# Kernel optimization log

Hardware: AMD Instinct MI355X
Metric: run time of the kernel (lower is better)

## Reference

```python
import jax, jax.numpy as jnp
import numpy as np

T, B, I_DIM, H_DIM = 256, 64, 1024, 1024


def setup_inputs() -> dict:
    key = jax.random.key(0)
    k_in, k_wx, k_wh = jax.random.split(key, 3)
    # xavier-normal-ish scale for [hidden, input] matrices
    std_x = float(np.sqrt(2.0 / (I_DIM + H_DIM)))
    std_h = float(np.sqrt(2.0 / (H_DIM + H_DIM)))
    return {
        "inputs": jax.random.normal(k_in, (T, B, I_DIM), dtype=jnp.float32),
        "W_x": jax.random.normal(k_wx, (4, H_DIM, I_DIM), dtype=jnp.float32) * std_x,
        "W_h": jax.random.normal(k_wh, (4, H_DIM, H_DIM), dtype=jnp.float32) * std_h,
        "bias": jnp.zeros((4, H_DIM), dtype=jnp.float32),
        "mask_x": jnp.ones((4, H_DIM, I_DIM), dtype=jnp.float32),
        "mask_h": jnp.ones((4, H_DIM, H_DIM), dtype=jnp.float32),
        "H0": jnp.zeros((B, H_DIM), dtype=jnp.float32),
        "C0": jnp.zeros((B, H_DIM), dtype=jnp.float32),
    }


def reference(inputs, W_x, W_h, bias, mask_x, mask_h, H0, C0):
    # masked + transposed weights: (4, in_dim, hidden) so X @ W works
    Wx_t = jnp.transpose(W_x * mask_x, (0, 2, 1))  # (4, I, H)
    Wh_t = jnp.transpose(W_h * mask_h, (0, 2, 1))  # (4, H, H)

    # gate order per original indexing: 0=i, 1=f, 2=o, 3=c
    def step(carry, X):
        H, C = carry
        # fused gate GEMMs: (4, B, H)
        g = (jnp.einsum('bi,gih->gbh', X, Wx_t)
             + jnp.einsum('bh,ghk->gbk', H, Wh_t)
             + bias[:, None, :])
        I_g = jax.nn.sigmoid(g[0])
        F_g = jax.nn.sigmoid(g[1])
        O_g = jax.nn.sigmoid(g[2])
        C_t = jnp.tanh(g[3])
        C_new = F_g * C + I_g * C_t
        H_new = O_g * jnp.tanh(C_new)
        return (H_new, C_new), H_new

    (_, _), outputs = jax.lax.scan(step, (H0, C0), inputs)
    return outputs  # (T, B, H)
```

## Files before the change

kernel.cpp:

```cpp
#include <hip/hip_runtime.h>

typedef __attribute__((ext_vector_type(8))) short short8;
typedef __attribute__((ext_vector_type(4))) float floatx4;

#define T_STEPS 256
#define BATCH   64
#define IDIM    1024
#define HDIM    1024
#define KDIM    (IDIM + HDIM)
#define MB      16
#define HB      16
#define NWG     256
#define NTHR    512
#define A_STRIDE (KDIM + 8)
#define FLAG_STRIDE 16

__device__ __forceinline__ unsigned short f2bf(float f) {
  unsigned u = __float_as_uint(f);
  u += 0x7FFFu + ((u >> 16) & 1u);
  return (unsigned short)(u >> 16);
}

__global__ void prep_weights(const float* __restrict__ Wx, const float* __restrict__ Wh,
                             const float* __restrict__ mx, const float* __restrict__ mh,
                             unsigned short* __restrict__ Wcat) {
  int idx = blockIdx.x * blockDim.x + threadIdx.x;
  const int total = 4 * HDIM * KDIM / 4;
  if (idx >= total) return;
  int k4 = idx & (KDIM / 4 - 1);
  int gh = idx >> 9;
  int k = k4 * 4;
  float4 v, m;
  if (k < IDIM) {
    v = *(const float4*)(Wx + (size_t)gh * IDIM + k);
    m = *(const float4*)(mx + (size_t)gh * IDIM + k);
  } else {
    v = *(const float4*)(Wh + (size_t)gh * HDIM + (k - IDIM));
    m = *(const float4*)(mh + (size_t)gh * HDIM + (k - IDIM));
  }
  ushort4 o;
  o.x = f2bf(v.x * m.x); o.y = f2bf(v.y * m.y);
  o.z = f2bf(v.z * m.z); o.w = f2bf(v.w * m.w);
  *(ushort4*)(Wcat + (size_t)gh * KDIM + k) = o;
}

__global__ void prep_h0(const float* __restrict__ H0, unsigned short* __restrict__ Hbuf0,
                        unsigned* __restrict__ flags) {
  int i = blockIdx.x * blockDim.x + threadIdx.x;
  if (i < BATCH * HDIM) Hbuf0[i] = f2bf(H0[i]);
  if (i < 4 * 64 * FLAG_STRIDE) flags[i] = 0u;
}

__global__ void __launch_bounds__(NTHR, 2)
lstm_main(const float* __restrict__ X,
          const float* __restrict__ bias,
          const float* __restrict__ C0,
          const unsigned short* __restrict__ Wcat,
          unsigned short* __restrict__ Hbuf0,
          unsigned short* __restrict__ Hbuf1,
          unsigned* __restrict__ flags,
          float* __restrict__ out)
{
  __shared__ __align__(16) unsigned short Ash[MB * A_STRIDE];
  __shared__ float parts[4][MB][HB + 1];

  const int tid  = threadIdx.x;
  const int wg   = blockIdx.x;
  const int bg   = wg >> 6;
  const int hg   = wg & 63;
  const int b0   = bg * MB;
  const int h0   = hg * HB;

  const int w    = tid >> 6;
  const int lane = tid & 63;
  const int nl   = lane & 15;
  const int quad = lane >> 4;

  short8 Bfr[4][8];
  {
    const short8* wp = (const short8*)Wcat;
#pragma unroll
    for (int g = 0; g < 4; ++g) {
      const int rowbase = (g * HDIM + h0 + nl) * (KDIM / 8);
#pragma unroll
      for (int ks = 0; ks < 8; ++ks)
        Bfr[g][ks] = wp[rowbase + w * 32 + ks * 4 + quad];
    }
  }

  float c_state = 0.f;
  const int eb = tid >> 4;
  const int eh = tid & 15;
  if (tid < 256) c_state = C0[(b0 + eb) * HDIM + h0 + eh];

  float* pflat = &parts[0][0][0];
  const int e0 = tid, e1 = tid + NTHR;
  const int p0 = (e0 >> 8) * (MB * (HB + 1)) + ((e0 >> 4) & 15) * (HB + 1) + (e0 & 15);
  const int p1 = (e1 >> 8) * (MB * (HB + 1)) + ((e1 >> 4) & 15) * (HB + 1) + (e1 & 15);
  const float binit0 = bias[(e0 >> 8) * HDIM + h0 + (e0 & 15)];
  const float binit1 = bias[(e1 >> 8) * HDIM + h0 + (e1 & 15)];

  unsigned* myflag = flags + (bg * 64 + hg) * FLAG_STRIDE;
  const int c8 = tid & 127;
  const int mrow = tid >> 7;
  unsigned* depflag = flags + (bg * 64 + (c8 >> 1)) * FLAG_STRIDE;

  for (int t = 0; t < T_STEPS; ++t) {
    const unsigned short* __restrict__ Hprev = (t & 1) ? Hbuf1 : Hbuf0;
    unsigned short* __restrict__ Hnext       = (t & 1) ? Hbuf0 : Hbuf1;

    {
      const float4* xp = (const float4*)(X + ((size_t)t * BATCH + b0) * IDIM);
#pragma unroll
      for (int it = 0; it < (MB * IDIM / 4) / NTHR; ++it) {
        int v = it * NTHR + tid;
        int m = v >> 8;
        int c4 = v & 255;
        float4 f = xp[m * (IDIM / 4) + c4];
        ushort4 o;
        o.x = f2bf(f.x); o.y = f2bf(f.y); o.z = f2bf(f.z); o.w = f2bf(f.w);
        *(ushort4*)&Ash[m * A_STRIDE + c4 * 4] = o;
      }
    }
    pflat[p0] = binit0;
    pflat[p1] = binit1;

    {
      const unsigned tgt = (unsigned)t;
      while (__hip_atomic_load(depflag, __ATOMIC_RELAXED,
                               __HIP_MEMORY_SCOPE_AGENT) < tgt) {
        __builtin_amdgcn_s_sleep(1);
      }
    }

    {
      const unsigned short* pa = Hprev + (size_t)(b0 + mrow) * HDIM + c8 * 8;
      uint4 d0, d1, d2, d3;
      asm volatile(
        "global_load_dwordx4 %0, %4, off sc0 sc1\n\t"
        "global_load_dwordx4 %1, %5, off sc0 sc1\n\t"
        "global_load_dwordx4 %2, %6, off sc0 sc1\n\t"
        "global_load_dwordx4 %3, %7, off sc0 sc1\n\t"
        "s_waitcnt vmcnt(0)"
        : "=&v"(d0), "=&v"(d1), "=&v"(d2), "=&v"(d3)
        : "v"(pa), "v"(pa + 4 * HDIM), "v"(pa + 8 * HDIM), "v"(pa + 12 * HDIM)
        : "memory");
      *(uint4*)&Ash[(mrow +  0) * A_STRIDE + IDIM + c8 * 8] = d0;
      *(uint4*)&Ash[(mrow +  4) * A_STRIDE + IDIM + c8 * 8] = d1;
      *(uint4*)&Ash[(mrow +  8) * A_STRIDE + IDIM + c8 * 8] = d2;
      *(uint4*)&Ash[(mrow + 12) * A_STRIDE + IDIM + c8 * 8] = d3;
    }
    __syncthreads();

    floatx4 acc[4];
#pragma unroll
    for (int g = 0; g < 4; ++g) acc[g] = floatx4{0.f, 0.f, 0.f, 0.f};
    {
      const unsigned short* abase = &Ash[nl * A_STRIDE + w * 256 + quad * 8];
#pragma unroll
      for (int ks = 0; ks < 8; ++ks) {
        short8 af = *(const short8*)(abase + ks * 32);
#pragma unroll
        for (int g = 0; g < 4; ++g)
          acc[g] = __builtin_amdgcn_mfma_f32_16x16x32_bf16(af, Bfr[g][ks], acc[g], 0, 0, 0);
      }
    }
#pragma unroll
    for (int g = 0; g < 4; ++g)
#pragma unroll
      for (int r = 0; r < 4; ++r)
        atomicAdd(&parts[g][quad * 4 + r][nl], acc[g][r]);
    __syncthreads();

    if (tid < 256) {
      float gI = parts[0][eb][eh];
      float gF = parts[1][eb][eh];
      float gO = parts[2][eb][eh];
      float gC = parts[3][eb][eh];
      float ig = 1.f / (1.f + __expf(-gI));
      float fg = 1.f / (1.f + __expf(-gF));
      float og = 1.f / (1.f + __expf(-gO));
      float cb = 1.f - 2.f / (__expf(2.f * gC) + 1.f);
      c_state = fg * c_state + ig * cb;
      float hn = og * (1.f - 2.f / (__expf(2.f * c_state) + 1.f));
      out[((size_t)t * BATCH + b0 + eb) * HDIM + h0 + eh] = hn;
      unsigned short hb = f2bf(hn);
      unsigned short* ps = Hnext + (size_t)(b0 + eb) * HDIM + h0 + eh;
      asm volatile("global_store_short %0, %1, off sc0 sc1"
                   :: "v"(ps), "v"((unsigned)hb) : "memory");
    }
    asm volatile("s_waitcnt vmcnt(0)" ::: "memory");
    __syncthreads();
    if (tid == 0) {
      __hip_atomic_store(myflag, (unsigned)(t + 1), __ATOMIC_RELAXED,
                         __HIP_MEMORY_SCOPE_AGENT);
    }
  }
}

extern "C" void kernel_launch(void* const* d_in, const int* in_sizes, int n_in,
                              void* d_out, int out_size, void* d_ws, size_t ws_size,
                              hipStream_t stream) {
  const float* X    = (const float*)d_in[0];
  const float* Wx   = (const float*)d_in[1];
  const float* Wh   = (const float*)d_in[2];
  const float* bias = (const float*)d_in[3];
  const float* mx   = (const float*)d_in[4];
  const float* mh   = (const float*)d_in[5];
  const float* H0   = (const float*)d_in[6];
  const float* C0   = (const float*)d_in[7];
  float* out = (float*)d_out;

  unsigned short* Wcat  = (unsigned short*)d_ws;
  unsigned short* Hbuf0 = Wcat + (size_t)4 * HDIM * KDIM;
  unsigned short* Hbuf1 = Hbuf0 + BATCH * HDIM;
  unsigned*       flags = (unsigned*)(Hbuf1 + BATCH * HDIM);

  {
    int tot = 4 * HDIM * KDIM / 4;
    prep_weights<<<(tot + 255) / 256, 256, 0, stream>>>(Wx, Wh, mx, mh, Wcat);
  }
  prep_h0<<<(BATCH * HDIM + 255) / 256, 256, 0, stream>>>(H0, Hbuf0, flags);

  void* args[] = { (void*)&X, (void*)&bias, (void*)&C0, (void*)&Wcat,
                   (void*)&Hbuf0, (void*)&Hbuf1, (void*)&flags, (void*)&out };
  hipLaunchCooperativeKernel(reinterpret_cast<void*>(lstm_main),
                             dim3(NWG), dim3(NTHR), args, 0, stream);
}
```

Before: 3.627 ms.

## Replace per-block flags with sharded counters and prefetch next-step inputs into registers

Each block used to spin (every thread) on the flag of the producer block owning its H columns. Now a single thread polls four sharded atomic counters per batch group until all 64 blocks of that group have finished the step, then releases the block with a barrier. The next timestep's X slice is loaded into registers during the MFMA phase, so its global latency overlaps compute. The partial-sum buffer is double-buffered, and the output store is moved after the H store. Risks are contention from many blocks atomically incrementing the same counters, and extra register pressure from the prefetch.

```diff
diff --git a/kernel.cpp b/kernel.cpp
--- a/kernel.cpp
+++ b/kernel.cpp
@@ -13,7 +13,6 @@
 #define NWG     256
 #define NTHR    512
 #define A_STRIDE (KDIM + 8)
-#define FLAG_STRIDE 16
 
 __device__ __forceinline__ unsigned short f2bf(float f) {
   unsigned u = __float_as_uint(f);
@@ -45,10 +44,10 @@
 }
 
 __global__ void prep_h0(const float* __restrict__ H0, unsigned short* __restrict__ Hbuf0,
-                        unsigned* __restrict__ flags) {
+                        unsigned* __restrict__ cnt) {
   int i = blockIdx.x * blockDim.x + threadIdx.x;
   if (i < BATCH * HDIM) Hbuf0[i] = f2bf(H0[i]);
-  if (i < 4 * 64 * FLAG_STRIDE) flags[i] = 0u;
+  if (i < 16 * 16) cnt[i] = 0u;
 }
 
 __global__ void __launch_bounds__(NTHR, 2)
@@ -58,11 +57,11 @@
           const unsigned short* __restrict__ Wcat,
           unsigned short* __restrict__ Hbuf0,
           unsigned short* __restrict__ Hbuf1,
-          unsigned* __restrict__ flags,
+          unsigned* __restrict__ cnt,
           float* __restrict__ out)
 {
   __shared__ __align__(16) unsigned short Ash[MB * A_STRIDE];
-  __shared__ float parts[4][MB][HB + 1];
+  __shared__ float parts[2][4][MB][HB + 1];
 
   const int tid  = threadIdx.x;
   const int wg   = blockIdx.x;
@@ -93,45 +92,57 @@
   const int eh = tid & 15;
   if (tid < 256) c_state = C0[(b0 + eb) * HDIM + h0 + eh];
 
-  float* pflat = &parts[0][0][0];
   const int e0 = tid, e1 = tid + NTHR;
   const int p0 = (e0 >> 8) * (MB * (HB + 1)) + ((e0 >> 4) & 15) * (HB + 1) + (e0 & 15);
   const int p1 = (e1 >> 8) * (MB * (HB + 1)) + ((e1 >> 4) & 15) * (HB + 1) + (e1 & 15);
   const float binit0 = bias[(e0 >> 8) * HDIM + h0 + (e0 & 15)];
   const float binit1 = bias[(e1 >> 8) * HDIM + h0 + (e1 & 15)];
 
-  unsigned* myflag = flags + (bg * 64 + hg) * FLAG_STRIDE;
   const int c8 = tid & 127;
   const int mrow = tid >> 7;
-  unsigned* depflag = flags + (bg * 64 + (c8 >> 1)) * FLAG_STRIDE;
+
+  unsigned* mycnt  = cnt + (bg * 4 + (hg & 3)) * 16;
+  unsigned* bgcnt  = cnt + bg * 4 * 16;
+
+  float4 Xpre[8];
+  {
+    const float4* xp = (const float4*)(X + (size_t)b0 * IDIM);
+#pragma unroll
+    for (int it = 0; it < 8; ++it) {
+      int v = it * NTHR + tid;
+      Xpre[it] = xp[(v >> 8) * (IDIM / 4) + (v & 255)];
+    }
+  }
 
   for (int t = 0; t < T_STEPS; ++t) {
     const unsigned short* __restrict__ Hprev = (t & 1) ? Hbuf1 : Hbuf0;
     unsigned short* __restrict__ Hnext       = (t & 1) ? Hbuf0 : Hbuf1;
-
-    {
-      const float4* xp = (const float4*)(X + ((size_t)t * BATCH + b0) * IDIM);
-#pragma unroll
-      for (int it = 0; it < (MB * IDIM / 4) / NTHR; ++it) {
-        int v = it * NTHR + tid;
-        int m = v >> 8;
-        int c4 = v & 255;
-        float4 f = xp[m * (IDIM / 4) + c4];
-        ushort4 o;
-        o.x = f2bf(f.x); o.y = f2bf(f.y); o.z = f2bf(f.z); o.w = f2bf(f.w);
-        *(ushort4*)&Ash[m * A_STRIDE + c4 * 4] = o;
+    float* pcur = &parts[t & 1][0][0][0];
+
+#pragma unroll
+    for (int it = 0; it < 8; ++it) {
+      int v = it * NTHR + tid;
+      int m = v >> 8, c4 = v & 255;
+      float4 f = Xpre[it];
+      ushort4 o;
+      o.x = f2bf(f.x); o.y = f2bf(f.y); o.z = f2bf(f.z); o.w = f2bf(f.w);
+      *(ushort4*)&Ash[m * A_STRIDE + c4 * 4] = o;
+    }
+    pcur[p0] = binit0;
+    pcur[p1] = binit1;
+
+    if (tid == 0 && t > 0) {
+      const unsigned tgt = (unsigned)(64 * t);
+      for (;;) {
+        unsigned s = __hip_atomic_load(bgcnt +  0, __ATOMIC_RELAXED, __HIP_MEMORY_SCOPE_AGENT)
+                   + __hip_atomic_load(bgcnt + 16, __ATOMIC_RELAXED, __HIP_MEMORY_SCOPE_AGENT)
+                   + __hip_atomic_load(bgcnt + 32, __ATOMIC_RELAXED, __HIP_MEMORY_SCOPE_AGENT)
+                   + __hip_atomic_load(bgcnt + 48, __ATOMIC_RELAXED, __HIP_MEMORY_SCOPE_AGENT);
+        if (s >= tgt) break;
+        __builtin_amdgcn_s_sleep(8);
       }
     }
-    pflat[p0] = binit0;
-    pflat[p1] = binit1;
-
-    {
-      const unsigned tgt = (unsigned)t;
-      while (__hip_atomic_load(depflag, __ATOMIC_RELAXED,
-                               __HIP_MEMORY_SCOPE_AGENT) < tgt) {
-        __builtin_amdgcn_s_sleep(1);
-      }
-    }
+    __syncthreads();
 
     {
       const unsigned short* pa = Hprev + (size_t)(b0 + mrow) * HDIM + c8 * 8;
@@ -152,6 +163,16 @@
     }
     __syncthreads();
 
+    {
+      int tn = (t + 1 < T_STEPS) ? t + 1 : t;
+      const float4* xp = (const float4*)(X + ((size_t)tn * BATCH + b0) * IDIM);
+#pragma unroll
+      for (int it = 0; it < 8; ++it) {
+        int v = it * NTHR + tid;
+        Xpre[it] = xp[(v >> 8) * (IDIM / 4) + (v & 255)];
+      }
+    }
+
     floatx4 acc[4];
 #pragma unroll
     for (int g = 0; g < 4; ++g) acc[g] = floatx4{0.f, 0.f, 0.f, 0.f};
@@ -169,32 +190,29 @@
     for (int g = 0; g < 4; ++g)
 #pragma unroll
       for (int r = 0; r < 4; ++r)
-        atomicAdd(&parts[g][quad * 4 + r][nl], acc[g][r]);
+        atomicAdd(&parts[t & 1][g][quad * 4 + r][nl], acc[g][r]);
     __syncthreads();
 
     if (tid < 256) {
-      float gI = parts[0][eb][eh];
-      float gF = parts[1][eb][eh];
-      float gO = parts[2][eb][eh];
-      float gC = parts[3][eb][eh];
+      float gI = parts[t & 1][0][eb][eh];
+      float gF = parts[t & 1][1][eb][eh];
+      float gO = parts[t & 1][2][eb][eh];
+      float gC = parts[t & 1][3][eb][eh];
       float ig = 1.f / (1.f + __expf(-gI));
       float fg = 1.f / (1.f + __expf(-gF));
       float og = 1.f / (1.f + __expf(-gO));
       float cb = 1.f - 2.f / (__expf(2.f * gC) + 1.f);
       c_state = fg * c_state + ig * cb;
       float hn = og * (1.f - 2.f / (__expf(2.f * c_state) + 1.f));
-      out[((size_t)t * BATCH + b0 + eb) * HDIM + h0 + eh] = hn;
       unsigned short hb = f2bf(hn);
       unsigned short* ps = Hnext + (size_t)(b0 + eb) * HDIM + h0 + eh;
       asm volatile("global_store_short %0, %1, off sc0 sc1"
                    :: "v"(ps), "v"((unsigned)hb) : "memory");
+      out[((size_t)t * BATCH + b0 + eb) * HDIM + h0 + eh] = hn;
     }
     asm volatile("s_waitcnt vmcnt(0)" ::: "memory");
     __syncthreads();
-    if (tid == 0) {
-      __hip_atomic_store(myflag, (unsigned)(t + 1), __ATOMIC_RELAXED,
-                         __HIP_MEMORY_SCOPE_AGENT);
-    }
+    if (tid == 0) atomicAdd(mycnt, 1u);
   }
 }
 
@@ -214,16 +232,16 @@
   unsigned short* Wcat  = (unsigned short*)d_ws;
   unsigned short* Hbuf0 = Wcat + (size_t)4 * HDIM * KDIM;
   unsigned short* Hbuf1 = Hbuf0 + BATCH * HDIM;
-  unsigned*       flags = (unsigned*)(Hbuf1 + BATCH * HDIM);
+  unsigned*       cnt   = (unsigned*)(Hbuf1 + BATCH * HDIM);
 
   {
     int tot = 4 * HDIM * KDIM / 4;
     prep_weights<<<(tot + 255) / 256, 256, 0, stream>>>(Wx, Wh, mx, mh, Wcat);
   }
-  prep_h0<<<(BATCH * HDIM + 255) / 256, 256, 0, stream>>>(H0, Hbuf0, flags);
+  prep_h0<<<(BATCH * HDIM + 255) / 256, 256, 0, stream>>>(H0, Hbuf0, cnt);
 
   void* args[] = { (void*)&X, (void*)&bias, (void*)&C0, (void*)&Wcat,
-                   (void*)&Hbuf0, (void*)&Hbuf1, (void*)&flags, (void*)&out };
+                   (void*)&Hbuf0, (void*)&Hbuf1, (void*)&cnt, (void*)&out };
   hipLaunchCooperativeKernel(reinterpret_cast<void*>(lstm_main),
                              dim3(NWG), dim3(NTHR), args, 0, stream);
 }
```

After: 3.475 ms. -4.2%, faster.
